# Kernel tuning notes

Measured on AMD Instinct MI355X. Metric: run time of the kernel, lower is better.

## Reference

```python
import jax, jax.numpy as jnp
import numpy as np

S = 4096      # keystrokes
H = 32        # hidden_dim / d_model
NH = 8        # nhead
HD = H // NH  # head dim = 4
FF = 2048     # torch TransformerEncoderLayer default dim_feedforward
NL = 6        # num_layers
EPS = 1e-5


def setup_inputs() -> dict:
    key = jax.random.key(0)
    ks = jax.random.split(key, 20)
    sc = 0.02
    ts = jnp.sort(jax.random.uniform(ks[0], (S,), minval=0.0, maxval=2.49e7))
    feats = jax.random.normal(ks[1], (S, 2), dtype=jnp.float32)
    data = jnp.concatenate([ts[:, None], feats], axis=1)  # [S, 3]
    return {
        "data": data,
        "lin_w": jax.random.normal(ks[2], (H, 2)) * sc,
        "lin_b": jnp.zeros((H,)),
        "qkv_w": jax.random.normal(ks[3], (NL, 3 * H, H)) * sc,
        "qkv_b": jnp.zeros((NL, 3 * H)),
        "out_w": jax.random.normal(ks[4], (NL, H, H)) * sc,
        "out_b": jnp.zeros((NL, H)),
        "ln1_g": jnp.ones((NL, H)),
        "ln1_b": jnp.zeros((NL, H)),
        "ff1_w": jax.random.normal(ks[5], (NL, FF, H)) * sc,
        "ff1_b": jnp.zeros((NL, FF)),
        "ff2_w": jax.random.normal(ks[6], (NL, H, FF)) * sc,
        "ff2_b": jnp.zeros((NL, H)),
        "ln2_g": jnp.ones((NL, H)),
        "ln2_b": jnp.zeros((NL, H)),
        "cls_w": jax.random.normal(ks[7], (1, H)) * sc,
        "cls_b": jnp.zeros((1,)),
    }


def _ln(x, g, b):
    m = x.mean(-1, keepdims=True)
    v = ((x - m) ** 2).mean(-1, keepdims=True)
    return (x - m) / jnp.sqrt(v + EPS) * g + b


def reference(data, lin_w, lin_b, qkv_w, qkv_b, out_w, out_b,
              ln1_g, ln1_b, ff1_w, ff1_b, ff2_w, ff2_b,
              ln2_g, ln2_b, cls_w, cls_b):
    # per-keystroke Linear+ReLU, vectorized over the sequence
    x = jax.nn.relu(data[:, 1:] @ lin_w.T + lin_b)            # [S, H]
    # sinusoidal time encoding at index timestamp//100
    ts_idx = (data[:, 0] / 100.0).astype(jnp.int32)            # [S]
    div = jnp.exp(jnp.arange(0, H, 2, dtype=jnp.float32) * (-np.log(10000.0) / H))
    ang = ts_idx[:, None].astype(jnp.float32) * div            # [S, H/2]
    pe = jnp.stack([jnp.sin(ang), jnp.cos(ang)], axis=-1).reshape(S, H)
    x = x + pe
    # prepend CLS token of -1.0 -> seq len S+1
    x = jnp.concatenate([jnp.full((1, H), -1.0, dtype=x.dtype), x], axis=0)
    L = S + 1
    for i in range(NL):  # post-LN encoder layers (torch defaults, eval/no-dropout)
        qkv = x @ qkv_w[i].T + qkv_b[i]                        # [L, 3H]
        q, k, v = jnp.split(qkv, 3, axis=-1)
        q = q.reshape(L, NH, HD)
        k = k.reshape(L, NH, HD)
        v = v.reshape(L, NH, HD)
        scores = jnp.einsum('qhd,khd->hqk', q, k) / np.sqrt(HD)
        attn = jax.nn.softmax(scores, axis=-1)                 # [NH, L, L]
        o = jnp.einsum('hqk,khd->qhd', attn, v).reshape(L, H)
        o = o @ out_w[i].T + out_b[i]
        x = _ln(x + o, ln1_g[i], ln1_b[i])
        f = jax.nn.relu(x @ ff1_w[i].T + ff1_b[i]) @ ff2_w[i].T + ff2_b[i]
        x = _ln(x + f, ln2_g[i], ln2_b[i])
    cls_out = x[0]                                             # [H]
    return jax.nn.sigmoid(cls_out @ cls_w.T + cls_b)           # [1]
```

## Files before the change

### kernel.cpp

```cpp
#include <hip/hip_runtime.h>
#include <hip/hip_bf16.h>
#include <math.h>

#define SEQ 4096
#define LL  4097
#define HDIM 32
#define FFD 2048
#define NLAYER 6
#define EPSLN 1e-5f
#define NCHUNK 16
#define KPAD 4128
#define QROWS 4352
#define RB2 16
#define LB 32

#if __has_builtin(__builtin_amdgcn_exp2f)
#define EXP2 __builtin_amdgcn_exp2f
#else
#define EXP2 exp2f
#endif

#define QSCALE 0.7213475204444817f

typedef short bf16x8 __attribute__((ext_vector_type(8)));
typedef short bf16x4 __attribute__((ext_vector_type(4)));
typedef float f32x4 __attribute__((ext_vector_type(4)));

__device__ __forceinline__ unsigned short f2b(float f) {
  unsigned int b = __float_as_uint(f);
  b += 0x7FFFu + ((b >> 16) & 1u);
  return (unsigned short)(b >> 16);
}

__device__ __forceinline__ float b2f(unsigned short u) {
  unsigned int b = ((unsigned int)u) << 16;
  return __uint_as_float(b);
}

__device__ __forceinline__ unsigned int pk_bf16(float a, float b) {
  __hip_bfloat162 h = __float22bfloat162_rn(make_float2(a, b));
  return *(unsigned int*)&h;
}

__device__ __forceinline__ f32x4 mfma_qk(bf16x4 a, bf16x4 b, f32x4 c) {
#if __has_builtin(__builtin_amdgcn_mfma_f32_16x16x16bf16_1k)
  return __builtin_amdgcn_mfma_f32_16x16x16bf16_1k(a, b, c, 0, 0, 0);
#else
  bf16x8 a8 = {a[0], a[1], a[2], a[3], 0, 0, 0, 0};
  bf16x8 b8 = {b[0], b[1], b[2], b[3], 0, 0, 0, 0};
  return __builtin_amdgcn_mfma_f32_16x16x32_bf16(a8, b8, c, 0, 0, 0);
#endif
}


__device__ __forceinline__ void qkv_wave(float y, int row, bool ok, int lane,
    const float* __restrict__ qw, const float* __restrict__ qb,
    unsigned short* __restrict__ Qb, unsigned short* __restrict__ KB4,
    unsigned short* __restrict__ VB5) {
  int ch = lane & 31;
  float xv[32];
#pragma unroll
  for (int k = 0; k < 32; ++k) xv[k] = __shfl(y, (lane & 32) + k, 64);
#pragma unroll
  for (int t3 = 0; t3 < 3; ++t3) {
    int cc = t3 * 32 + ch;
    const float4* wr = (const float4*)(qw + (size_t)cc * 32);
    float acc = qb[cc];
#pragma unroll
    for (int k8 = 0; k8 < 8; ++k8) {
      float4 wv = wr[k8];
      acc = fmaf(xv[4 * k8 + 0], wv.x, acc);
      acc = fmaf(xv[4 * k8 + 1], wv.y, acc);
      acc = fmaf(xv[4 * k8 + 2], wv.z, acc);
      acc = fmaf(xv[4 * k8 + 3], wv.w, acc);
    }
    if (ok) {
      int h = ch >> 2;
      if (t3 == 0) {
        Qb[(size_t)row * 32 + ch] = f2b(QSCALE * acc);
      } else if (t3 == 1) {
        KB4[((size_t)h * KPAD + row) * 4 + (ch & 3)] = f2b(acc);
      } else {
        int w = row & 31;
        int pos = ((w & 15) << 1) | (w >> 4);
        VB5[((size_t)h * 5 + (ch & 3)) * KPAD + (row & ~31) + pos] = f2b(acc);
      }
    }
  }
}

__global__ __launch_bounds__(256) void k_init(const float* __restrict__ data,
    const float* __restrict__ lin_w, const float* __restrict__ lin_b,
    const float* __restrict__ qkv_w, const float* __restrict__ qkv_b,
    const float* __restrict__ ff1_w, const float* __restrict__ ff2_w,
    float* __restrict__ X, unsigned short* __restrict__ Qb,
    unsigned short* __restrict__ KB4, unsigned short* __restrict__ VB5,
    unsigned short* __restrict__ W1B, unsigned short* __restrict__ W2B) {
  int gid = blockIdx.x * 256 + threadIdx.x;
  int gsz = gridDim.x * 256;
  const int NW = NLAYER * FFD * 32;
  for (int i = gid; i < NW; i += gsz) {
    W1B[i] = f2b(ff1_w[i]);
    W2B[i] = f2b(ff2_w[i]);
  }
  for (int i = gid; i < (QROWS - LL) * 32; i += gsz)
    Qb[(size_t)LL * 32 + i] = 0;
  for (int i = gid; i < 8 * (KPAD - LL) * 4; i += gsz) {
    int hh = i / ((KPAD - LL) * 4);
    int rem = i % ((KPAD - LL) * 4);
    KB4[((size_t)hh * KPAD + LL) * 4 + rem] = 0;
  }
  for (int i = gid; i < 8 * 5 * KPAD; i += gsz) {
    int col = i % KPAD;
    int dd = (i / KPAD) % 5;
    if (dd == 4) {
      int key = (col & ~31) + ((col & 1) << 4) + ((col & 31) >> 1);
      VB5[i] = (key <= 4096) ? 0x3F80 : 0;
    } else if (col > 4096) {
      VB5[i] = 0;
    }
  }
  int wave = threadIdx.x >> 6, lane = threadIdx.x & 63;
  int r = lane >> 5, ch = lane & 31;
  unsigned wgid = blockIdx.x * 4 + wave;
  for (unsigned it = wgid; it < 2049; it += gridDim.x * 4) {
    int row = it * 2 + r;
    bool ok = row < LL;
    float val = 0.f;
    if (ok) {
      if (row == 0) {
        val = -1.0f;
      } else {
        int s = row - 1;
        float ts = data[s * 3 + 0];
        float f0 = data[s * 3 + 1];
        float f1 = data[s * 3 + 2];
        float lin = f0 * lin_w[ch * 2 + 0] + f1 * lin_w[ch * 2 + 1] + lin_b[ch];
        lin = fmaxf(lin, 0.0f);
        int tsi = (int)(ts / 100.0f);
        int j = ch >> 1;
        float aj = (float)(2 * j) * (float)(-0.28782313662425575);
        float divj = (float)exp((double)aj);
        float ang = (float)tsi * divj;
        float pe = (ch & 1) ? cosf(ang) : sinf(ang);
        val = lin + pe;
      }
      X[(size_t)row * HDIM + ch] = val;
    }
    qkv_wave(val, row, ok, lane, qkv_w, qkv_b, Qb, KB4, VB5);
  }
}

__global__ __launch_bounds__(256, 4) void k_attn(
    const unsigned short* __restrict__ Qb, const unsigned short* __restrict__ KB4,
    const unsigned short* __restrict__ VB5, float* __restrict__ LP,
    float4* __restrict__ AP4) {
  int tid = threadIdx.x;
  int wave = tid >> 6, lane = tid & 63;
  int l16 = lane & 15, quad = lane >> 4;
  int h = blockIdx.y, c = blockIdx.z;
  int qs = blockIdx.x * 4 + wave;
  if (qs >= 65) return;
  int q0 = qs * 64;
  int kb0 = c * 256;
  int nkb = (c == NCHUNK - 1) ? 9 : 8;

  const unsigned short* KBh = KB4 + (size_t)h * KPAD * 4;
  const unsigned short* VBh = VB5 + (size_t)h * 5 * KPAD;
  const bool kl = (quad == (h & 3));
  const bool vl = (l16 < 5);
  const int qcol0 = (h >> 2) * 16 + quad * 4;

  bf16x4 aq[4];
#pragma unroll
  for (int t = 0; t < 4; ++t)
    aq[t] = *(const bf16x4*)&Qb[(size_t)(q0 + t * 16 + l16) * 32 + qcol0];

  const bf16x4 zb4 = {0, 0, 0, 0};
  const bf16x8 zb8 = {0, 0, 0, 0, 0, 0, 0, 0};
  f32x4 acc0[4], acc1[4];
#pragma unroll
  for (int t = 0; t < 4; ++t) {
    acc0[t] = (f32x4){0.f, 0.f, 0.f, 0.f};
    acc1[t] = (f32x4){0.f, 0.f, 0.f, 0.f};
  }

  auto step = [&](int k0, f32x4* acc) {
    bf16x4 bk0 = kl ? *(const bf16x4*)&KBh[(size_t)(k0 + l16) * 4] : zb4;
    bf16x4 bk1 = kl ? *(const bf16x4*)&KBh[(size_t)(k0 + 16 + l16) * 4] : zb4;
    bf16x8 bv = vl ? *(const bf16x8*)&VBh[(size_t)l16 * KPAD + k0 + quad * 8]
                   : zb8;
    f32x4 z = {0.f, 0.f, 0.f, 0.f};
    unsigned pf[4][4];
#pragma unroll
    for (int t = 0; t < 4; ++t) {
      f32x4 s0 = mfma_qk(bk0, aq[t], z);
      f32x4 s1 = mfma_qk(bk1, aq[t], z);
#pragma unroll
      for (int reg = 0; reg < 4; ++reg)
        pf[t][reg] = pk_bf16(EXP2(s0[reg]), EXP2(s1[reg]));
    }
#pragma unroll
    for (int t = 0; t < 4; ++t) {
      bf16x8 pb = *(const bf16x8*)&pf[t][0];
      acc[t] = __builtin_amdgcn_mfma_f32_16x16x32_bf16(bv, pb, acc[t], 0, 0, 0);
    }
  };

  int kb = 0;
  for (; kb + 2 <= nkb; kb += 2) {
    step(kb0 + kb * 32, acc0);
    step(kb0 + (kb + 1) * 32, acc1);
  }
  if (kb < nkb) step(kb0 + kb * 32, acc0);

#pragma unroll
  for (int t = 0; t < 4; ++t) {
    f32x4 a = acc0[t] + acc1[t];
    int q = q0 + t * 16 + l16;
    if (q < LL) {
      if (quad == 0) {
        AP4[((size_t)c * LL + q) * 8 + h] = make_float4(a[0], a[1], a[2], a[3]);
      } else if (quad == 1) {
        LP[((size_t)c * LL + q) * 8 + h] = a[0];
      }
    }
  }
}

__global__ __launch_bounds__(512, 4) void k_ffnF(const float* __restrict__ LP,
    const float* __restrict__ APf, float* __restrict__ X,
    const float* __restrict__ ow, const float* __restrict__ ob,
    const float* __restrict__ g1, const float* __restrict__ b1ln,
    const unsigned short* __restrict__ w1b, const float* __restrict__ fb1,
    const unsigned short* __restrict__ w2b, const float* __restrict__ fb2,
    const float* __restrict__ g2, const float* __restrict__ b2ln,
    const float* __restrict__ qw, const float* __restrict__ qb,
    unsigned short* __restrict__ Qb, unsigned short* __restrict__ KB4,
    unsigned short* __restrict__ VB5) {
  __shared__ unsigned short Xa[RB2][32];
  __shared__ float Y1[RB2][32];
  __shared__ unsigned short Fsb[8][16 * 136];
  __shared__ float Pr[8][RB2 * 33];
  int tid = threadIdx.x;
  int wave = tid >> 6, lane = tid & 63;
  int l16 = lane & 15, quad = lane >> 4;
  int r = lane >> 5, ch = lane & 31;
  int r0 = blockIdx.x * RB2;

  {
    int rl = wave * 2 + r;
    int row = r0 + rl;
    bool ok = row < LL;
    int hh = ch >> 2;
    float L = 0.f, A = 0.f;
    if (ok) {
#pragma unroll
      for (int c = 0; c < NCHUNK; ++c) {
        A += APf[((size_t)c * LL + row) * 32 + ch];
        L += LP[((size_t)c * LL + row) * 8 + hh];
      }
    }
    float os = ok ? A / L : 0.f;
    float acc = 0.f;
    const float4* owr = (const float4*)(ow + (size_t)ch * 32);
#pragma unroll
    for (int k8 = 0; k8 < 8; ++k8) {
      float4 wv = owr[k8];
      acc = fmaf(__shfl(os, (lane & 32) + 4 * k8 + 0, 64), wv.x, acc);
      acc = fmaf(__shfl(os, (lane & 32) + 4 * k8 + 1, 64), wv.y, acc);
      acc = fmaf(__shfl(os, (lane & 32) + 4 * k8 + 2, 64), wv.z, acc);
      acc = fmaf(__shfl(os, (lane & 32) + 4 * k8 + 3, 64), wv.w, acc);
    }
    float val = ok ? (X[(size_t)row * HDIM + ch] + acc + ob[ch]) : 0.f;
    float mean = val;
#pragma unroll
    for (int off = 16; off > 0; off >>= 1) mean += __shfl_xor(mean, off, 32);
    mean *= (1.f / 32.f);
    float d2 = val - mean;
    float var = d2 * d2;
#pragma unroll
    for (int off = 16; off > 0; off >>= 1) var += __shfl_xor(var, off, 32);
    var *= (1.f / 32.f);
    float y = d2 / sqrtf(var + EPSLN) * g1[ch] + b1ln[ch];
    Y1[rl][ch] = y;
    Xa[rl][ch] = ok ? f2b(y) : 0;
  }
  __syncthreads();

  bf16x8 a1 = *(const bf16x8*)&Xa[l16][quad * 8];
  f32x4 acc2[2] = {{0.f, 0.f, 0.f, 0.f}, {0.f, 0.f, 0.f, 0.f}};
  int fs0 = wave * 256;
#pragma unroll
  for (int sg = 0; sg < 2; ++sg) {
    int f0 = fs0 + sg * 128;
    f32x4 c1[8];
#pragma unroll
    for (int t = 0; t < 8; ++t) {
      bf16x8 b =
          *(const bf16x8*)&w1b[(size_t)(f0 + t * 16 + l16) * 32 + quad * 8];
      f32x4 z = {0.f, 0.f, 0.f, 0.f};
      c1[t] = __builtin_amdgcn_mfma_f32_16x16x32_bf16(a1, b, z, 0, 0, 0);
    }
#pragma unroll
    for (int t = 0; t < 8; ++t) {
      float bb = fb1[f0 + t * 16 + l16];
#pragma unroll
      for (int reg = 0; reg < 4; ++reg) {
        float v = fmaxf(c1[t][reg] + bb, 0.f);
        Fsb[wave][(quad * 4 + reg) * 136 + t * 16 + l16] = f2b(v);
      }
    }
#pragma unroll
    for (int kt = 0; kt < 4; ++kt) {
      bf16x8 a2 = *(const bf16x8*)&Fsb[wave][l16 * 136 + kt * 32 + quad * 8];
#pragma unroll
      for (int u = 0; u < 2; ++u) {
        bf16x8 b = *(const bf16x8*)&w2b[(size_t)(u * 16 + l16) * FFD + f0 +
                                        kt * 32 + quad * 8];
        acc2[u] =
            __builtin_amdgcn_mfma_f32_16x16x32_bf16(a2, b, acc2[u], 0, 0, 0);
      }
    }
  }
#pragma unroll
  for (int u = 0; u < 2; ++u)
#pragma unroll
    for (int reg = 0; reg < 4; ++reg)
      Pr[wave][(quad * 4 + reg) * 33 + u * 16 + l16] = acc2[u][reg];
  __syncthreads();

  {
    int rl = wave * 2 + r;
    int row = r0 + rl;
    bool ok = row < LL;
    float s = 0.f;
#pragma unroll
    for (int w = 0; w < 8; ++w) s += Pr[w][rl * 33 + ch];
    float val = ok ? (Y1[rl][ch] + s + fb2[ch]) : 0.f;
    float mean = val;
#pragma unroll
    for (int off = 16; off > 0; off >>= 1) mean += __shfl_xor(mean, off, 32);
    mean *= (1.f / 32.f);
    float d2 = val - mean;
    float var = d2 * d2;
#pragma unroll
    for (int off = 16; off > 0; off >>= 1) var += __shfl_xor(var, off, 32);
    var *= (1.f / 32.f);
    float y = d2 / sqrtf(var + EPSLN) * g2[ch] + b2ln[ch];
    if (ok) X[(size_t)row * HDIM + ch] = y;
    qkv_wave(y, row, ok, lane, qw, qb, Qb, KB4, VB5);
  }
}

__global__ __launch_bounds__(256) void k_lastB(const float* __restrict__ LP,
    const float* __restrict__ APf, const float* __restrict__ X,
    const float* __restrict__ ow, const float* __restrict__ ob,
    const float* __restrict__ g1, const float* __restrict__ b1ln,
    const unsigned short* __restrict__ w1b, const float* __restrict__ fb1,
    const unsigned short* __restrict__ w2b, float* __restrict__ y1_ws,
    float* __restrict__ part) {
  __shared__ float y1_sh[32];
  __shared__ float f_sh[64];
  __shared__ float red[8][32];
  int tid = threadIdx.x;
  int b = blockIdx.x;

  if (tid < 32) {
    int ch = tid, hh = ch >> 2;
    float A = 0.f, L = 0.f;
#pragma unroll
    for (int c = 0; c < NCHUNK; ++c) {
      A += APf[((size_t)c * LL) * 32 + ch];
      L += LP[((size_t)c * LL) * 8 + hh];
    }
    float os = A / L;
    float acc = 0.f;
#pragma unroll
    for (int k = 0; k < 32; ++k)
      acc = fmaf(__shfl(os, k, 32), ow[ch * 32 + k], acc);
    float val = X[ch] + acc + ob[ch];
    float mean = val;
#pragma unroll
    for (int off = 16; off > 0; off >>= 1) mean += __shfl_xor(mean, off, 32);
    mean *= (1.f / 32.f);
    float d2 = val - mean;
    float var = d2 * d2;
#pragma unroll
    for (int off = 16; off > 0; off >>= 1) var += __shfl_xor(var, off, 32);
    var *= (1.f / 32.f);
    float y = d2 / sqrtf(var + EPSLN) * g1[ch] + b1ln[ch];
    y1_sh[ch] = y;
    if (b == 0) y1_ws[ch] = y;
  }
  __syncthreads();

  if (tid < 64) {
    int i = b * 64 + tid;
    const unsigned short* wr = w1b + (size_t)i * 32;
    float acc = fb1[i];
#pragma unroll
    for (int j = 0; j < 32; ++j) acc = fmaf(y1_sh[j], b2f(wr[j]), acc);
    f_sh[tid] = fmaxf(acc, 0.f);
  }
  __syncthreads();

  {
    int ch = tid & 31, seg = tid >> 5;
    float acc = 0.f;
    const unsigned short* wr = w2b + (size_t)ch * FFD + b * 64 + seg * 8;
#pragma unroll
    for (int j = 0; j < 8; ++j) acc = fmaf(f_sh[seg * 8 + j], b2f(wr[j]), acc);
    red[seg][ch] = acc;
  }
  __syncthreads();
  if (tid < 32) {
    float s = 0.f;
#pragma unroll
    for (int sg = 0; sg < 8; ++sg) s += red[sg][tid];
    part[b * 32 + tid] = s;
  }
}

__global__ __launch_bounds__(64) void k_lastC(const float* __restrict__ y1_ws,
    const float* __restrict__ part, const float* __restrict__ fb2,
    const float* __restrict__ g2, const float* __restrict__ b2ln,
    const float* __restrict__ cw, const float* __restrict__ cb,
    float* __restrict__ out) {
  int tid = threadIdx.x;
  if (tid >= 32) return;
  int ch = tid;
  float s = 0.f;
#pragma unroll 4
  for (int b = 0; b < LB; ++b) s += part[b * 32 + ch];
  float val = y1_ws[ch] + s + fb2[ch];
  float mean = val;
#pragma unroll
  for (int off = 16; off > 0; off >>= 1) mean += __shfl_xor(mean, off, 32);
  mean *= (1.f / 32.f);
  float d2 = val - mean;
  float var = d2 * d2;
#pragma unroll
  for (int off = 16; off > 0; off >>= 1) var += __shfl_xor(var, off, 32);
  var *= (1.f / 32.f);
  float y = d2 / sqrtf(var + EPSLN) * g2[ch] + b2ln[ch];
  float t = y * cw[ch];
#pragma unroll
  for (int off = 16; off > 0; off >>= 1) t += __shfl_xor(t, off, 32);
  if (ch == 0) out[0] = 1.f / (1.f + expf(-(t + cb[0])));
}

extern "C" void kernel_launch(void* const* d_in, const int* in_sizes, int n_in,
                              void* d_out, int out_size, void* d_ws,
                              size_t ws_size, hipStream_t stream) {
  const float* data  = (const float*)d_in[0];
  const float* lin_w = (const float*)d_in[1];
  const float* lin_b = (const float*)d_in[2];
  const float* qkv_w = (const float*)d_in[3];
  const float* qkv_b = (const float*)d_in[4];
  const float* out_w = (const float*)d_in[5];
  const float* out_b = (const float*)d_in[6];
  const float* ln1_g = (const float*)d_in[7];
  const float* ln1_b = (const float*)d_in[8];
  const float* ff1_w = (const float*)d_in[9];
  const float* ff1_b = (const float*)d_in[10];
  const float* ff2_w = (const float*)d_in[11];
  const float* ff2_b = (const float*)d_in[12];
  const float* ln2_g = (const float*)d_in[13];
  const float* ln2_b = (const float*)d_in[14];
  const float* cls_w = (const float*)d_in[15];
  const float* cls_b = (const float*)d_in[16];

  char* wsb = (char*)d_ws;
  float* X = (float*)wsb;
  unsigned short* Qb  = (unsigned short*)(X + (size_t)LL * 32);
  unsigned short* KB4 = Qb + (size_t)QROWS * 32;
  unsigned short* VB5 = KB4 + (size_t)8 * KPAD * 4;
  unsigned short* W1B = VB5 + (size_t)8 * 5 * KPAD;
  unsigned short* W2B = W1B + (size_t)NLAYER * FFD * 32;
  float4* AP = (float4*)(((size_t)(W2B + (size_t)NLAYER * FFD * 32) + 15) &
                         ~(size_t)15);
  float* LP = (float*)(AP + (size_t)NCHUNK * LL * 8);
  float* Y1W = LP + (size_t)NCHUNK * LL * 8;
  float* PART = Y1W + 32;

  k_init<<<1024, 256, 0, stream>>>(data, lin_w, lin_b, qkv_w, qkv_b,
                                   ff1_w, ff2_w, X, Qb, KB4, VB5, W1B, W2B);
  for (int l = 0; l < NLAYER - 1; ++l) {
    k_attn<<<dim3(17, 8, NCHUNK), 256, 0, stream>>>(Qb, KB4, VB5, LP, AP);
    const float* qw = qkv_w + (size_t)(l + 1) * 96 * 32;
    const float* qb = qkv_b + (size_t)(l + 1) * 96;
    k_ffnF<<<(LL + RB2 - 1) / RB2, 512, 0, stream>>>(
        LP, (const float*)AP, X,
        out_w + (size_t)l * 32 * 32, out_b + (size_t)l * 32,
        ln1_g + (size_t)l * 32, ln1_b + (size_t)l * 32,
        W1B + (size_t)l * FFD * 32, ff1_b + (size_t)l * FFD,
        W2B + (size_t)l * FFD * 32, ff2_b + (size_t)l * 32,
        ln2_g + (size_t)l * 32, ln2_b + (size_t)l * 32,
        qw, qb, Qb, KB4, VB5);
  }
  {
    const int l = NLAYER - 1;
    k_attn<<<dim3(1, 8, NCHUNK), 256, 0, stream>>>(Qb, KB4, VB5, LP, AP);
    k_lastB<<<LB, 256, 0, stream>>>(
        LP, (const float*)AP, X,
        out_w + (size_t)l * 32 * 32, out_b + (size_t)l * 32,
        ln1_g + (size_t)l * 32, ln1_b + (size_t)l * 32,
        W1B + (size_t)l * FFD * 32, ff1_b + (size_t)l * FFD,
        W2B + (size_t)l * FFD * 32, Y1W, PART);
    k_lastC<<<1, 64, 0, stream>>>(Y1W, PART, ff2_b + (size_t)l * 32,
                                  ln2_g + (size_t)l * 32,
                                  ln2_b + (size_t)l * 32,
                                  cls_w, cls_b, (float*)d_out);
  }
}
```

Measured before the change: 367.4 us.

## Fuse attention into per-layer FFN kernel with double-buffered QKV

```diff
diff --git a/kernel.cpp b/kernel.cpp
--- a/kernel.cpp
+++ b/kernel.cpp
@@ -93,8 +93,11 @@
     const float* __restrict__ lin_w, const float* __restrict__ lin_b,
     const float* __restrict__ qkv_w, const float* __restrict__ qkv_b,
     const float* __restrict__ ff1_w, const float* __restrict__ ff2_w,
-    float* __restrict__ X, unsigned short* __restrict__ Qb,
-    unsigned short* __restrict__ KB4, unsigned short* __restrict__ VB5,
+    float* __restrict__ X,
+    unsigned short* __restrict__ Qb0, unsigned short* __restrict__ KB40,
+    unsigned short* __restrict__ VB50,
+    unsigned short* __restrict__ Qb1, unsigned short* __restrict__ KB41,
+    unsigned short* __restrict__ VB51,
     unsigned short* __restrict__ W1B, unsigned short* __restrict__ W2B) {
   int gid = blockIdx.x * 256 + threadIdx.x;
   int gsz = gridDim.x * 256;
@@ -103,21 +106,27 @@
     W1B[i] = f2b(ff1_w[i]);
     W2B[i] = f2b(ff2_w[i]);
   }
-  for (int i = gid; i < (QROWS - LL) * 32; i += gsz)
-    Qb[(size_t)LL * 32 + i] = 0;
+  for (int i = gid; i < (QROWS - LL) * 32; i += gsz) {
+    Qb0[(size_t)LL * 32 + i] = 0;
+    Qb1[(size_t)LL * 32 + i] = 0;
+  }
   for (int i = gid; i < 8 * (KPAD - LL) * 4; i += gsz) {
     int hh = i / ((KPAD - LL) * 4);
     int rem = i % ((KPAD - LL) * 4);
-    KB4[((size_t)hh * KPAD + LL) * 4 + rem] = 0;
+    KB40[((size_t)hh * KPAD + LL) * 4 + rem] = 0;
+    KB41[((size_t)hh * KPAD + LL) * 4 + rem] = 0;
   }
   for (int i = gid; i < 8 * 5 * KPAD; i += gsz) {
     int col = i % KPAD;
     int dd = (i / KPAD) % 5;
     if (dd == 4) {
       int key = (col & ~31) + ((col & 1) << 4) + ((col & 31) >> 1);
-      VB5[i] = (key <= 4096) ? 0x3F80 : 0;
+      unsigned short v = (key <= 4096) ? 0x3F80 : 0;
+      VB50[i] = v;
+      VB51[i] = v;
     } else if (col > 4096) {
-      VB5[i] = 0;
+      VB50[i] = 0;
+      VB51[i] = 0;
     }
   }
   int wave = threadIdx.x >> 6, lane = threadIdx.x & 63;
@@ -147,7 +156,176 @@
       }
       X[(size_t)row * HDIM + ch] = val;
     }
-    qkv_wave(val, row, ok, lane, qkv_w, qkv_b, Qb, KB4, VB5);
+    qkv_wave(val, row, ok, lane, qkv_w, qkv_b, Qb0, KB40, VB50);
+  }
+}
+
+__global__ __launch_bounds__(512, 4) void k_layer(
+    const unsigned short* __restrict__ Qi, const unsigned short* __restrict__ Ki,
+    const unsigned short* __restrict__ Vi, float* __restrict__ X,
+    const float* __restrict__ ow, const float* __restrict__ ob,
+    const float* __restrict__ g1, const float* __restrict__ b1ln,
+    const unsigned short* __restrict__ w1b, const float* __restrict__ fb1,
+    const unsigned short* __restrict__ w2b, const float* __restrict__ fb2,
+    const float* __restrict__ g2, const float* __restrict__ b2ln,
+    const float* __restrict__ qw, const float* __restrict__ qb,
+    unsigned short* __restrict__ Qo, unsigned short* __restrict__ Ko,
+    unsigned short* __restrict__ Vo) {
+  __shared__ float os_sh[RB2][32];
+  __shared__ unsigned short Xa[RB2][32];
+  __shared__ float Y1[RB2][32];
+  __shared__ unsigned short Fsb[8][16 * 136];
+  __shared__ float Pr[8][RB2 * 33];
+  int tid = threadIdx.x;
+  int wave = tid >> 6, lane = tid & 63;
+  int l16 = lane & 15, quad = lane >> 4;
+  int r = lane >> 5, ch = lane & 31;
+  int r0 = blockIdx.x * RB2;
+
+  {
+    const int h = wave;
+    const unsigned short* KBh = Ki + (size_t)h * KPAD * 4;
+    const unsigned short* VBh = Vi + (size_t)h * 5 * KPAD;
+    const bool kl = (quad == (h & 3));
+    const bool vl = (l16 < 5);
+    const int qcol0 = (h >> 2) * 16 + quad * 4;
+    bf16x4 aq = *(const bf16x4*)&Qi[(size_t)(r0 + l16) * 32 + qcol0];
+    const bf16x4 zb4 = {0, 0, 0, 0};
+    const bf16x8 zb8 = {0, 0, 0, 0, 0, 0, 0, 0};
+    f32x4 total = {0.f, 0.f, 0.f, 0.f};
+
+    auto step = [&](int k0, f32x4& acc) {
+      bf16x4 bk0 = kl ? *(const bf16x4*)&KBh[(size_t)(k0 + l16) * 4] : zb4;
+      bf16x4 bk1 = kl ? *(const bf16x4*)&KBh[(size_t)(k0 + 16 + l16) * 4] : zb4;
+      bf16x8 bv = vl ? *(const bf16x8*)&VBh[(size_t)l16 * KPAD + k0 + quad * 8]
+                     : zb8;
+      f32x4 z = {0.f, 0.f, 0.f, 0.f};
+      f32x4 s0 = mfma_qk(bk0, aq, z);
+      f32x4 s1 = mfma_qk(bk1, aq, z);
+      unsigned pf[4];
+#pragma unroll
+      for (int reg = 0; reg < 4; ++reg)
+        pf[reg] = pk_bf16(EXP2(s0[reg]), EXP2(s1[reg]));
+      bf16x8 pb = *(const bf16x8*)&pf[0];
+      acc = __builtin_amdgcn_mfma_f32_16x16x32_bf16(bv, pb, acc, 0, 0, 0);
+    };
+
+    for (int c = 0; c < NCHUNK; ++c) {
+      int kb0 = c * 256;
+      int nkb = (c == NCHUNK - 1) ? 9 : 8;
+      f32x4 a0 = {0.f, 0.f, 0.f, 0.f}, a1 = {0.f, 0.f, 0.f, 0.f};
+      int kb = 0;
+      for (; kb + 2 <= nkb; kb += 2) {
+        step(kb0 + kb * 32, a0);
+        step(kb0 + (kb + 1) * 32, a1);
+      }
+      if (kb < nkb) step(kb0 + kb * 32, a0);
+      f32x4 aa = a0 + a1;
+      total += aa;
+    }
+    float Lv = __shfl(total[0], 16 + l16, 64);
+    if (quad == 0) {
+#pragma unroll
+      for (int reg = 0; reg < 4; ++reg)
+        os_sh[l16][h * 4 + reg] = total[reg] / Lv;
+    }
+  }
+  __syncthreads();
+
+  {
+    int rl = wave * 2 + r;
+    int row = r0 + rl;
+    bool ok = row < LL;
+    float acc = 0.f;
+    const float4* owr = (const float4*)(ow + (size_t)ch * 32);
+#pragma unroll
+    for (int k8 = 0; k8 < 8; ++k8) {
+      float4 wv = owr[k8];
+      acc = fmaf(os_sh[rl][4 * k8 + 0], wv.x, acc);
+      acc = fmaf(os_sh[rl][4 * k8 + 1], wv.y, acc);
+      acc = fmaf(os_sh[rl][4 * k8 + 2], wv.z, acc);
+      acc = fmaf(os_sh[rl][4 * k8 + 3], wv.w, acc);
+    }
+    float val = ok ? (X[(size_t)row * HDIM + ch] + acc + ob[ch]) : 0.f;
+    float mean = val;
+#pragma unroll
+    for (int off = 16; off > 0; off >>= 1) mean += __shfl_xor(mean, off, 32);
+    mean *= (1.f / 32.f);
+    float d2 = val - mean;
+    float var = d2 * d2;
+#pragma unroll
+    for (int off = 16; off > 0; off >>= 1) var += __shfl_xor(var, off, 32);
+    var *= (1.f / 32.f);
+    float y = d2 / sqrtf(var + EPSLN) * g1[ch] + b1ln[ch];
+    Y1[rl][ch] = y;
+    Xa[rl][ch] = ok ? f2b(y) : 0;
+  }
+  __syncthreads();
+
+  {
+    bf16x8 a1 = *(const bf16x8*)&Xa[l16][quad * 8];
+    f32x4 acc2[2] = {{0.f, 0.f, 0.f, 0.f}, {0.f, 0.f, 0.f, 0.f}};
+    int fs0 = wave * 256;
+#pragma unroll
+    for (int sg = 0; sg < 2; ++sg) {
+      int f0 = fs0 + sg * 128;
+      f32x4 c1[8];
+#pragma unroll
+      for (int t = 0; t < 8; ++t) {
+        bf16x8 b =
+            *(const bf16x8*)&w1b[(size_t)(f0 + t * 16 + l16) * 32 + quad * 8];
+        f32x4 z = {0.f, 0.f, 0.f, 0.f};
+        c1[t] = __builtin_amdgcn_mfma_f32_16x16x32_bf16(a1, b, z, 0, 0, 0);
+      }
+#pragma unroll
+      for (int t = 0; t < 8; ++t) {
+        float bb = fb1[f0 + t * 16 + l16];
+#pragma unroll
+        for (int reg = 0; reg < 4; ++reg) {
+          float v = fmaxf(c1[t][reg] + bb, 0.f);
+          Fsb[wave][(quad * 4 + reg) * 136 + t * 16 + l16] = f2b(v);
+        }
+      }
+#pragma unroll
+      for (int kt = 0; kt < 4; ++kt) {
+        bf16x8 a2 = *(const bf16x8*)&Fsb[wave][l16 * 136 + kt * 32 + quad * 8];
+#pragma unroll
+        for (int u = 0; u < 2; ++u) {
+          bf16x8 b = *(const bf16x8*)&w2b[(size_t)(u * 16 + l16) * FFD + f0 +
+                                          kt * 32 + quad * 8];
+          acc2[u] =
+              __builtin_amdgcn_mfma_f32_16x16x32_bf16(a2, b, acc2[u], 0, 0, 0);
+        }
+      }
+    }
+#pragma unroll
+    for (int u = 0; u < 2; ++u)
+#pragma unroll
+      for (int reg = 0; reg < 4; ++reg)
+        Pr[wave][(quad * 4 + reg) * 33 + u * 16 + l16] = acc2[u][reg];
+  }
+  __syncthreads();
+
+  {
+    int rl = wave * 2 + r;
+    int row = r0 + rl;
+    bool ok = row < LL;
+    float s = 0.f;
+#pragma unroll
+    for (int w = 0; w < 8; ++w) s += Pr[w][rl * 33 + ch];
+    float val = ok ? (Y1[rl][ch] + s + fb2[ch]) : 0.f;
+    float mean = val;
+#pragma unroll
+    for (int off = 16; off > 0; off >>= 1) mean += __shfl_xor(mean, off, 32);
+    mean *= (1.f / 32.f);
+    float d2 = val - mean;
+    float var = d2 * d2;
+#pragma unroll
+    for (int off = 16; off > 0; off >>= 1) var += __shfl_xor(var, off, 32);
+    var *= (1.f / 32.f);
+    float y = d2 / sqrtf(var + EPSLN) * g2[ch] + b2ln[ch];
+    if (ok) X[(size_t)row * HDIM + ch] = y;
+    qkv_wave(y, row, ok, lane, qw, qb, Qo, Ko, Vo);
   }
 }
 
@@ -225,131 +403,6 @@
         LP[((size_t)c * LL + q) * 8 + h] = a[0];
       }
     }
-  }
-}
-
-__global__ __launch_bounds__(512, 4) void k_ffnF(const float* __restrict__ LP,
-    const float* __restrict__ APf, float* __restrict__ X,
-    const float* __restrict__ ow, const float* __restrict__ ob,
-    const float* __restrict__ g1, const float* __restrict__ b1ln,
-    const unsigned short* __restrict__ w1b, const float* __restrict__ fb1,
-    const unsigned short* __restrict__ w2b, const float* __restrict__ fb2,
-    const float* __restrict__ g2, const float* __restrict__ b2ln,
-    const float* __restrict__ qw, const float* __restrict__ qb,
-    unsigned short* __restrict__ Qb, unsigned short* __restrict__ KB4,
-    unsigned short* __restrict__ VB5) {
-  __shared__ unsigned short Xa[RB2][32];
-  __shared__ float Y1[RB2][32];
-  __shared__ unsigned short Fsb[8][16 * 136];
-  __shared__ float Pr[8][RB2 * 33];
-  int tid = threadIdx.x;
-  int wave = tid >> 6, lane = tid & 63;
-  int l16 = lane & 15, quad = lane >> 4;
-  int r = lane >> 5, ch = lane & 31;
-  int r0 = blockIdx.x * RB2;
-
-  {
-    int rl = wave * 2 + r;
-    int row = r0 + rl;
-    bool ok = row < LL;
-    int hh = ch >> 2;
-    float L = 0.f, A = 0.f;
-    if (ok) {
-#pragma unroll
-      for (int c = 0; c < NCHUNK; ++c) {
-        A += APf[((size_t)c * LL + row) * 32 + ch];
-        L += LP[((size_t)c * LL + row) * 8 + hh];
-      }
-    }
-    float os = ok ? A / L : 0.f;
-    float acc = 0.f;
-    const float4* owr = (const float4*)(ow + (size_t)ch * 32);
-#pragma unroll
-    for (int k8 = 0; k8 < 8; ++k8) {
-      float4 wv = owr[k8];
-      acc = fmaf(__shfl(os, (lane & 32) + 4 * k8 + 0, 64), wv.x, acc);
-      acc = fmaf(__shfl(os, (lane & 32) + 4 * k8 + 1, 64), wv.y, acc);
-      acc = fmaf(__shfl(os, (lane & 32) + 4 * k8 + 2, 64), wv.z, acc);
-      acc = fmaf(__shfl(os, (lane & 32) + 4 * k8 + 3, 64), wv.w, acc);
-    }
-    float val = ok ? (X[(size_t)row * HDIM + ch] + acc + ob[ch]) : 0.f;
-    float mean = val;
-#pragma unroll
-    for (int off = 16; off > 0; off >>= 1) mean += __shfl_xor(mean, off, 32);
-    mean *= (1.f / 32.f);
-    float d2 = val - mean;
-    float var = d2 * d2;
-#pragma unroll
-    for (int off = 16; off > 0; off >>= 1) var += __shfl_xor(var, off, 32);
-    var *= (1.f / 32.f);
-    float y = d2 / sqrtf(var + EPSLN) * g1[ch] + b1ln[ch];
-    Y1[rl][ch] = y;
-    Xa[rl][ch] = ok ? f2b(y) : 0;
-  }
-  __syncthreads();
-
-  bf16x8 a1 = *(const bf16x8*)&Xa[l16][quad * 8];
-  f32x4 acc2[2] = {{0.f, 0.f, 0.f, 0.f}, {0.f, 0.f, 0.f, 0.f}};
-  int fs0 = wave * 256;
-#pragma unroll
-  for (int sg = 0; sg < 2; ++sg) {
-    int f0 = fs0 + sg * 128;
-    f32x4 c1[8];
-#pragma unroll
-    for (int t = 0; t < 8; ++t) {
-      bf16x8 b =
-          *(const bf16x8*)&w1b[(size_t)(f0 + t * 16 + l16) * 32 + quad * 8];
-      f32x4 z = {0.f, 0.f, 0.f, 0.f};
-      c1[t] = __builtin_amdgcn_mfma_f32_16x16x32_bf16(a1, b, z, 0, 0, 0);
-    }
-#pragma unroll
-    for (int t = 0; t < 8; ++t) {
-      float bb = fb1[f0 + t * 16 + l16];
-#pragma unroll
-      for (int reg = 0; reg < 4; ++reg) {
-        float v = fmaxf(c1[t][reg] + bb, 0.f);
-        Fsb[wave][(quad * 4 + reg) * 136 + t * 16 + l16] = f2b(v);
-      }
-    }
-#pragma unroll
-    for (int kt = 0; kt < 4; ++kt) {
-      bf16x8 a2 = *(const bf16x8*)&Fsb[wave][l16 * 136 + kt * 32 + quad * 8];
-#pragma unroll
-      for (int u = 0; u < 2; ++u) {
-        bf16x8 b = *(const bf16x8*)&w2b[(size_t)(u * 16 + l16) * FFD + f0 +
-                                        kt * 32 + quad * 8];
-        acc2[u] =
-            __builtin_amdgcn_mfma_f32_16x16x32_bf16(a2, b, acc2[u], 0, 0, 0);
-      }
-    }
-  }
-#pragma unroll
-  for (int u = 0; u < 2; ++u)
-#pragma unroll
-    for (int reg = 0; reg < 4; ++reg)
-      Pr[wave][(quad * 4 + reg) * 33 + u * 16 + l16] = acc2[u][reg];
-  __syncthreads();
-
-  {
-    int rl = wave * 2 + r;
-    int row = r0 + rl;
-    bool ok = row < LL;
-    float s = 0.f;
-#pragma unroll
-    for (int w = 0; w < 8; ++w) s += Pr[w][rl * 33 + ch];
-    float val = ok ? (Y1[rl][ch] + s + fb2[ch]) : 0.f;
-    float mean = val;
-#pragma unroll
-    for (int off = 16; off > 0; off >>= 1) mean += __shfl_xor(mean, off, 32);
-    mean *= (1.f / 32.f);
-    float d2 = val - mean;
-    float var = d2 * d2;
-#pragma unroll
-    for (int off = 16; off > 0; off >>= 1) var += __shfl_xor(var, off, 32);
-    var *= (1.f / 32.f);
-    float y = d2 / sqrtf(var + EPSLN) * g2[ch] + b2ln[ch];
-    if (ok) X[(size_t)row * HDIM + ch] = y;
-    qkv_wave(y, row, ok, lane, qw, qb, Qb, KB4, VB5);
   }
 }
 
@@ -473,10 +526,13 @@
 
   char* wsb = (char*)d_ws;
   float* X = (float*)wsb;
-  unsigned short* Qb  = (unsigned short*)(X + (size_t)LL * 32);
-  unsigned short* KB4 = Qb + (size_t)QROWS * 32;
-  unsigned short* VB5 = KB4 + (size_t)8 * KPAD * 4;
-  unsigned short* W1B = VB5 + (size_t)8 * 5 * KPAD;
+  unsigned short* Qb0 = (unsigned short*)(X + (size_t)LL * 32);
+  unsigned short* KB40 = Qb0 + (size_t)QROWS * 32;
+  unsigned short* VB50 = KB40 + (size_t)8 * KPAD * 4;
+  unsigned short* Qb1 = VB50 + (size_t)8 * 5 * KPAD;
+  unsigned short* KB41 = Qb1 + (size_t)QROWS * 32;
+  unsigned short* VB51 = KB41 + (size_t)8 * KPAD * 4;
+  unsigned short* W1B = VB51 + (size_t)8 * 5 * KPAD;
   unsigned short* W2B = W1B + (size_t)NLAYER * FFD * 32;
   float4* AP = (float4*)(((size_t)(W2B + (size_t)NLAYER * FFD * 32) + 15) &
                          ~(size_t)15);
@@ -484,24 +540,29 @@
   float* Y1W = LP + (size_t)NCHUNK * LL * 8;
   float* PART = Y1W + 32;
 
+  unsigned short* Qs[2] = {Qb0, Qb1};
+  unsigned short* Ks[2] = {KB40, KB41};
+  unsigned short* Vs[2] = {VB50, VB51};
+
   k_init<<<1024, 256, 0, stream>>>(data, lin_w, lin_b, qkv_w, qkv_b,
-                                   ff1_w, ff2_w, X, Qb, KB4, VB5, W1B, W2B);
+                                   ff1_w, ff2_w, X, Qb0, KB40, VB50,
+                                   Qb1, KB41, VB51, W1B, W2B);
   for (int l = 0; l < NLAYER - 1; ++l) {
-    k_attn<<<dim3(17, 8, NCHUNK), 256, 0, stream>>>(Qb, KB4, VB5, LP, AP);
+    int in = l & 1, outp = (l + 1) & 1;
     const float* qw = qkv_w + (size_t)(l + 1) * 96 * 32;
     const float* qb = qkv_b + (size_t)(l + 1) * 96;
-    k_ffnF<<<(LL + RB2 - 1) / RB2, 512, 0, stream>>>(
-        LP, (const float*)AP, X,
+    k_layer<<<(LL + RB2 - 1) / RB2, 512, 0, stream>>>(
+        Qs[in], Ks[in], Vs[in], X,
         out_w + (size_t)l * 32 * 32, out_b + (size_t)l * 32,
         ln1_g + (size_t)l * 32, ln1_b + (size_t)l * 32,
         W1B + (size_t)l * FFD * 32, ff1_b + (size_t)l * FFD,
         W2B + (size_t)l * FFD * 32, ff2_b + (size_t)l * 32,
         ln2_g + (size_t)l * 32, ln2_b + (size_t)l * 32,
-        qw, qb, Qb, KB4, VB5);
+        qw, qb, Qs[outp], Ks[outp], Vs[outp]);
   }
   {
     const int l = NLAYER - 1;
-    k_attn<<<dim3(1, 8, NCHUNK), 256, 0, stream>>>(Qb, KB4, VB5, LP, AP);
+    k_attn<<<dim3(1, 8, NCHUNK), 256, 0, stream>>>(Qs[1], Ks[1], Vs[1], LP, AP);
     k_lastB<<<LB, 256, 0, stream>>>(
         LP, (const float*)AP, X,
         out_w + (size_t)l * 32 * 32, out_b + (size_t)l * 32,
```

Result: slower. 509.3 us (+38.6%).
